# Kernel tuning notes

Measured on AMD Instinct MI355X. Metric: run time of the kernel, lower is better.

Reference implementation:

```python
import jax, jax.numpy as jnp
import numpy as np


def setup_inputs() -> dict:
    key = jax.random.key(0)
    k1, k2 = jax.random.split(key)
    n_tokens, hidden, n_experts = 16384, 3072, 64
    activations = jax.random.normal(k1, (n_tokens, hidden), dtype=jnp.float32)
    logits = jax.random.normal(k2, (n_tokens, n_experts), dtype=jnp.float32)
    capacity = 256  # int(capacity_factor * n_tokens / n_experts) with capacity_factor=1.0
    return {"activations": activations, "logits": logits, "capacity": capacity}


def reference(activations, logits, capacity):
    """Top-1 MoE gating + capacity-limited token dispatch (DeepSpeed MoEGating, top_k=1).

    Returns (moe_input, scores, expert_assignment, mapped_slots, expert_counts).
    Dispatched rows are pre-scaled by the gate score (fused scale-and-scatter).
    """
    n_tokens, hidden = activations.shape
    n_experts = logits.shape[1]

    probs = jax.nn.softmax(logits, axis=-1)                       # [T, E], fp32
    expert = jnp.argmax(logits, axis=-1)                          # [T]
    mask1 = jax.nn.one_hot(expert, n_experts, dtype=jnp.int32)    # [T, E]

    # position of each token within its chosen expert's allocation
    locations = jnp.cumsum(mask1, axis=0) - 1                     # [T, E]
    loc_s = jnp.sum(locations * mask1, axis=1)                    # [T]

    keep = loc_s < capacity                                       # capacity-based dropping
    score = jnp.take_along_axis(probs, expert[:, None], axis=1)[:, 0]
    score = jnp.where(keep, score, 0.0)

    # dispatch buffer size, padded to a multiple of 256 (matches kernel path)
    size = n_experts * capacity
    if size % 256 != 0:
        size = size + (256 - size % 256)

    slots = expert * capacity + loc_s                             # [T]
    slots_scatter = jnp.where(keep, slots, size)                  # OOB index -> dropped

    moe_input = jnp.zeros((size, hidden), dtype=activations.dtype)
    moe_input = moe_input.at[slots_scatter].set(
        activations * score[:, None].astype(activations.dtype), mode="drop")

    expert_assignment = expert.astype(jnp.int32)
    mapped_slots = jnp.where(keep, slots, -1).astype(jnp.int32)
    expert_counts = jnp.sum(mask1 * keep[:, None].astype(jnp.int32), axis=0).astype(jnp.int32)

    return moe_input, score, expert_assignment, mapped_slots, expert_counts
```

## Files before the change

### kernel.cpp

```cpp
#include <hip/hip_runtime.h>

#define T_TOKENS 16384
#define HIDDEN   3072
#define NEXP     64
#define CAP      256
#define BLK      256
#define NGB      (T_TOKENS / BLK)
#define DSIZE    (NEXP * CAP)
#define NW       (BLK / 64)

__global__ __launch_bounds__(BLK) void gate_kernel(
    const float* __restrict__ logits,
    int* __restrict__ expertOut, int* __restrict__ rankOut,
    float* __restrict__ scoreOut, int* __restrict__ histOut) {
  __shared__ int wcnt[NW][NEXP];

  const int tid  = (int)threadIdx.x;
  const int lane = tid & 63;
  const int w    = tid >> 6;
  const int t    = blockIdx.x * BLK + tid;

  const float4* lg = (const float4*)(logits + (size_t)t * NEXP);
  float l[NEXP];
#pragma unroll
  for (int i = 0; i < NEXP / 4; ++i) {
    float4 v = lg[i];
    l[4 * i + 0] = v.x; l[4 * i + 1] = v.y;
    l[4 * i + 2] = v.z; l[4 * i + 3] = v.w;
  }

  float mx = l[0];
  int arg = 0;
#pragma unroll
  for (int i = 1; i < NEXP; ++i)
    if (l[i] > mx) { mx = l[i]; arg = i; }
  float s = 0.f;
#pragma unroll
  for (int i = 0; i < NEXP; ++i) s += __expf(l[i] - mx);
  const float score = 1.0f / s;

  ((int*)wcnt)[tid] = 0;
  __syncthreads();

  unsigned long long m = ~0ull;
#pragma unroll
  for (int b = 0; b < 6; ++b) {
    unsigned long long bal = __ballot((arg >> b) & 1);
    m &= ((arg >> b) & 1) ? bal : ~bal;
  }
  const unsigned long long ltm = (1ull << lane) - 1ull;
  const int rankInWave = __popcll(m & ltm);
  const bool leader = (__ffsll((unsigned long long)m) - 1) == lane;
  if (leader) wcnt[w][arg] = __popcll(m);
  __syncthreads();

  int r = rankInWave;
#pragma unroll
  for (int w2 = 0; w2 < NW; ++w2)
    if (w2 < w) r += wcnt[w2][arg];

  expertOut[t] = arg;
  rankOut[t]   = r;
  scoreOut[t]  = score;
  if (tid < NEXP) {
    int h = 0;
#pragma unroll
    for (int w2 = 0; w2 < NW; ++w2) h += wcnt[w2][tid];
    histOut[blockIdx.x * NEXP + tid] = h;
  }
}

__global__ __launch_bounds__(BLK) void finalize_kernel(
    const int* __restrict__ hist, const int* __restrict__ expert,
    const int* __restrict__ rank, const float* __restrict__ score,
    int* __restrict__ srcmap, float* __restrict__ sscore,
    int* __restrict__ kcnt,
    float* __restrict__ scoreOut, float* __restrict__ assignOut,
    float* __restrict__ slotsOut, float* __restrict__ countsOut) {
  __shared__ int h[NGB * NEXP];
  __shared__ int baseSh[NEXP];

  const int tid = (int)threadIdx.x;
  const int b   = (int)blockIdx.x;

  for (int i = tid; i < NGB * NEXP; i += BLK) h[i] = hist[i];
  __syncthreads();

  if (tid < NEXP) {
    int base = 0, tot = 0;
    for (int b2 = 0; b2 < NGB; ++b2) {
      int c = h[b2 * NEXP + tid];
      if (b2 < b) base += c;
      tot += c;
    }
    baseSh[tid] = base;
    if (b == 0) {
      int kc = min(tot, CAP);
      kcnt[tid] = kc;
      countsOut[tid] = (float)kc;
    }
  }
  __syncthreads();

  const int t   = b * BLK + tid;
  const int e   = expert[t];
  const int loc = baseSh[e] + rank[t];
  const float s = score[t];
  const bool keep = loc < CAP;

  scoreOut[t]  = keep ? s : 0.0f;
  assignOut[t] = (float)e;
  slotsOut[t]  = keep ? (float)(e * CAP + loc) : -1.0f;
  if (keep) {
    const int slot = e * CAP + loc;
    srcmap[slot] = t;
    sscore[slot] = s;
  }
}

__global__ __launch_bounds__(BLK) void scatter_kernel(
    const float* __restrict__ act, const int* __restrict__ srcmap,
    const float* __restrict__ sscore, const int* __restrict__ kcnt,
    float* __restrict__ moe) {
  const int i   = (int)blockIdx.x;
  const int e   = i >> 8;
  const int pos = i & (CAP - 1);

  float4* dst = (float4*)(moe + (size_t)i * HIDDEN);
  if (pos < kcnt[e]) {
    const int t   = srcmap[i];
    const float s = sscore[i];
    const float4* src = (const float4*)(act + (size_t)t * HIDDEN);
#pragma unroll
    for (int k = threadIdx.x; k < HIDDEN / 4; k += BLK) {
      float4 v = src[k];
      v.x *= s; v.y *= s; v.z *= s; v.w *= s;
      dst[k] = v;
    }
  } else {
    const float4 z = make_float4(0.f, 0.f, 0.f, 0.f);
#pragma unroll
    for (int k = threadIdx.x; k < HIDDEN / 4; k += BLK) dst[k] = z;
  }
}

extern "C" void kernel_launch(void* const* d_in, const int* in_sizes, int n_in,
                              void* d_out, int out_size, void* d_ws, size_t ws_size,
                              hipStream_t stream) {
  const float* act    = (const float*)d_in[0];
  const float* logits = (const float*)d_in[1];

  float* out       = (float*)d_out;
  float* moe       = out;
  float* scoreOut  = out + (size_t)DSIZE * HIDDEN;
  float* assignOut = scoreOut + T_TOKENS;
  float* slotsOut  = assignOut + T_TOKENS;
  float* countsOut = slotsOut + T_TOKENS;

  int*   expert = (int*)d_ws;
  int*   rank   = expert + T_TOKENS;
  float* score  = (float*)(rank + T_TOKENS);
  int*   hist   = (int*)(score + T_TOKENS);
  int*   kcnt   = hist + NGB * NEXP;
  int*   srcmap = kcnt + NEXP;
  float* sscore = (float*)(srcmap + DSIZE);

  gate_kernel<<<NGB, BLK, 0, stream>>>(logits, expert, rank, score, hist);
  finalize_kernel<<<NGB, BLK, 0, stream>>>(hist, expert, rank, score,
                                           srcmap, sscore, kcnt,
                                           scoreOut, assignOut, slotsOut,
                                           countsOut);
  scatter_kernel<<<DSIZE, BLK, 0, stream>>>(act, srcmap, sscore, kcnt, moe);
}
```

Before: 351.8 us.

## Batch scatter rows per block with nontemporal loads/stores and sentinel srcmap

The scatter kernel now handles 8 dispatch rows per block and prefetches their source indices up front. Row copies use nontemporal vector loads and stores so the large streaming traffic bypasses cache retention. The per-expert kept-count array is dropped: the gate kernel initialises srcmap to -1, and the scatter kernel zero-fills any row whose entry is still negative. This removes a dependent kcnt read and cuts the block count, in exchange for fewer, heavier blocks.

Result: faster. 341.2 us (-3.0%).

```diff
diff --git a/kernel.cpp b/kernel.cpp
--- a/kernel.cpp
+++ b/kernel.cpp
@@ -8,11 +8,15 @@
 #define NGB      (T_TOKENS / BLK)
 #define DSIZE    (NEXP * CAP)
 #define NW       (BLK / 64)
+#define RPB      8
+
+typedef float f4 __attribute__((ext_vector_type(4)));
 
 __global__ __launch_bounds__(BLK) void gate_kernel(
     const float* __restrict__ logits,
     int* __restrict__ expertOut, int* __restrict__ rankOut,
-    float* __restrict__ scoreOut, int* __restrict__ histOut) {
+    float* __restrict__ scoreOut, int* __restrict__ histOut,
+    int* __restrict__ srcmap) {
   __shared__ int wcnt[NW][NEXP];
 
   const int tid  = (int)threadIdx.x;
@@ -20,11 +24,13 @@
   const int w    = tid >> 6;
   const int t    = blockIdx.x * BLK + tid;
 
-  const float4* lg = (const float4*)(logits + (size_t)t * NEXP);
+  srcmap[t] = -1;
+
+  const f4* lg = (const f4*)(logits + (size_t)t * NEXP);
   float l[NEXP];
 #pragma unroll
   for (int i = 0; i < NEXP / 4; ++i) {
-    float4 v = lg[i];
+    f4 v = lg[i];
     l[4 * i + 0] = v.x; l[4 * i + 1] = v.y;
     l[4 * i + 2] = v.z; l[4 * i + 3] = v.w;
   }
@@ -74,7 +80,6 @@
     const int* __restrict__ hist, const int* __restrict__ expert,
     const int* __restrict__ rank, const float* __restrict__ score,
     int* __restrict__ srcmap, float* __restrict__ sscore,
-    int* __restrict__ kcnt,
     float* __restrict__ scoreOut, float* __restrict__ assignOut,
     float* __restrict__ slotsOut, float* __restrict__ countsOut) {
   __shared__ int h[NGB * NEXP];
@@ -94,11 +99,7 @@
       tot += c;
     }
     baseSh[tid] = base;
-    if (b == 0) {
-      int kc = min(tot, CAP);
-      kcnt[tid] = kc;
-      countsOut[tid] = (float)kc;
-    }
+    if (b == 0) countsOut[tid] = (float)min(tot, CAP);
   }
   __syncthreads();
 
@@ -120,27 +121,33 @@
 
 __global__ __launch_bounds__(BLK) void scatter_kernel(
     const float* __restrict__ act, const int* __restrict__ srcmap,
-    const float* __restrict__ sscore, const int* __restrict__ kcnt,
-    float* __restrict__ moe) {
-  const int i   = (int)blockIdx.x;
-  const int e   = i >> 8;
-  const int pos = i & (CAP - 1);
+    const float* __restrict__ sscore, float* __restrict__ moe) {
+  const int tid  = (int)threadIdx.x;
+  const int base = (int)blockIdx.x * RPB;
 
-  float4* dst = (float4*)(moe + (size_t)i * HIDDEN);
-  if (pos < kcnt[e]) {
-    const int t   = srcmap[i];
-    const float s = sscore[i];
-    const float4* src = (const float4*)(act + (size_t)t * HIDDEN);
+  int src[RPB];
 #pragma unroll
-    for (int k = threadIdx.x; k < HIDDEN / 4; k += BLK) {
-      float4 v = src[k];
-      v.x *= s; v.y *= s; v.z *= s; v.w *= s;
-      dst[k] = v;
+  for (int r = 0; r < RPB; ++r) src[r] = srcmap[base + r];
+
+#pragma unroll
+  for (int r = 0; r < RPB; ++r) {
+    const int row = base + r;
+    f4* dst = (f4*)(moe + (size_t)row * HIDDEN);
+    if (src[r] >= 0) {
+      const float s = sscore[row];
+      const f4* sp = (const f4*)(act + (size_t)src[r] * HIDDEN);
+#pragma unroll
+      for (int k = 0; k < HIDDEN / 4 / BLK; ++k) {
+        f4 v = __builtin_nontemporal_load(&sp[tid + k * BLK]);
+        v *= s;
+        __builtin_nontemporal_store(v, &dst[tid + k * BLK]);
+      }
+    } else {
+      const f4 z = {0.f, 0.f, 0.f, 0.f};
+#pragma unroll
+      for (int k = 0; k < HIDDEN / 4 / BLK; ++k)
+        __builtin_nontemporal_store(z, &dst[tid + k * BLK]);
     }
-  } else {
-    const float4 z = make_float4(0.f, 0.f, 0.f, 0.f);
-#pragma unroll
-    for (int k = threadIdx.x; k < HIDDEN / 4; k += BLK) dst[k] = z;
   }
 }
 
@@ -161,14 +168,14 @@
   int*   rank   = expert + T_TOKENS;
   float* score  = (float*)(rank + T_TOKENS);
   int*   hist   = (int*)(score + T_TOKENS);
-  int*   kcnt   = hist + NGB * NEXP;
-  int*   srcmap = kcnt + NEXP;
+  int*   srcmap = hist + NGB * NEXP;
   float* sscore = (float*)(srcmap + DSIZE);
 
-  gate_kernel<<<NGB, BLK, 0, stream>>>(logits, expert, rank, score, hist);
+  gate_kernel<<<NGB, BLK, 0, stream>>>(logits, expert, rank, score, hist,
+                                       srcmap);
   finalize_kernel<<<NGB, BLK, 0, stream>>>(hist, expert, rank, score,
-                                           srcmap, sscore, kcnt,
+                                           srcmap, sscore,
                                            scoreOut, assignOut, slotsOut,
                                            countsOut);
-  scatter_kernel<<<DSIZE, BLK, 0, stream>>>(act, srcmap, sscore, kcnt, moe);
+  scatter_kernel<<<DSIZE / RPB, BLK, 0, stream>>>(act, srcmap, sscore, moe);
 }
```
